# Optimization experiments

Hardware: AMD Instinct MI355X
Metric: run time of the kernel (lower is better)

Reference implementation:

```python
import jax, jax.numpy as jnp
import numpy as np


def setup_inputs() -> dict:
    key = jax.random.key(0)
    k0, k1, k2, k3, k4 = jax.random.split(key, 5)
    B, S, D, F, E = 2, 1024, 1024, 2048, 8
    x = jax.random.normal(k0, (B, S, D), dtype=jnp.float32)
    router_weight = jax.random.normal(k1, (D, E), dtype=jnp.float32) * (1.0 / np.sqrt(D))
    std_in = (1.0 / np.sqrt(3.0)) / np.sqrt(D)   # fan_in = d_model for w1/w2
    std_out = (1.0 / np.sqrt(3.0)) / np.sqrt(F)  # fan_in = d_ff for w3
    w1 = jax.random.normal(k2, (E, D, F), dtype=jnp.float32) * std_in
    w2 = jax.random.normal(k3, (E, D, F), dtype=jnp.float32) * std_in
    w3 = jax.random.normal(k4, (E, F, D), dtype=jnp.float32) * std_out
    return {"x": x, "router_weight": router_weight, "w1": w1, "w2": w2, "w3": w3, "top_k": 2}


def reference(x, router_weight, w1, w2, w3, top_k):
    B, S, D = x.shape
    E = w1.shape[0]
    xf = x.reshape(-1, D)                         # (T, D), T = B*S
    T = xf.shape[0]
    # Router: linear + softmax + top-k, then renormalize top-k weights
    logits = xf @ router_weight                   # (T, E)
    probs = jax.nn.softmax(logits, axis=-1)
    topk_w, topk_idx = jax.lax.top_k(probs, top_k)  # (T, k)
    topk_w = topk_w / jnp.sum(topk_w, axis=-1, keepdims=True)
    # Dense combine weights: cw[t, e] = routing weight if expert e selected for token t, else 0
    cw = jnp.zeros((T, E), dtype=xf.dtype).at[jnp.arange(T)[:, None], topk_idx].add(topk_w)
    # Expert SwiGLU: loop over small fixed expert count (structurally distinct weights)
    out = jnp.zeros_like(xf)
    for e in range(E):
        h = jax.nn.silu(xf @ w1[e]) * (xf @ w2[e])  # (T, F)
        out = out + cw[:, e:e + 1] * (h @ w3[e])    # (T, D)
    return out.reshape(B, S, D)
```

## Files before the change

kernel.cpp:

```cpp
#include <hip/hip_runtime.h>
#include <hip/hip_bf16.h>
#include <stdint.h>

#define T_TOK 2048
#define DMODEL 1024
#define FDIM 2048
#define NEXP 8
#define MAXS 40

typedef __bf16 bf16;
typedef __attribute__((ext_vector_type(8))) __bf16 bf16x8;
typedef __attribute__((ext_vector_type(4))) float f32x4;

#define GLOBAL_AS __attribute__((address_space(1)))
#define LDS_AS __attribute__((address_space(3)))

__global__ __launch_bounds__(64) void moe_router(
    const float* __restrict__ x, const float* __restrict__ rw,
    bf16* __restrict__ xb, int* __restrict__ counts,
    int* __restrict__ tok_list, float* __restrict__ wgt_list)
{
  const int t = blockIdx.x;
  const int lane = threadIdx.x;
  const float* xr = x + (size_t)t * DMODEL;
  bf16* xbr = xb + (size_t)t * DMODEL;
  float acc[NEXP];
#pragma unroll
  for (int e = 0; e < NEXP; ++e) acc[e] = 0.f;
  for (int d = lane; d < DMODEL; d += 64) {
    float xv = xr[d];
    xbr[d] = (bf16)xv;
    const float* r = rw + (size_t)d * NEXP;
#pragma unroll
    for (int e = 0; e < NEXP; ++e) acc[e] += xv * r[e];
  }
#pragma unroll
  for (int e = 0; e < NEXP; ++e) {
#pragma unroll
    for (int off = 32; off >= 1; off >>= 1)
      acc[e] += __shfl_xor(acc[e], off, 64);
  }
  if (lane == 0) {
    int i0 = 0; float m0 = acc[0];
#pragma unroll
    for (int e = 1; e < NEXP; ++e) { if (acc[e] > m0) { m0 = acc[e]; i0 = e; } }
    int i1 = -1; float m1 = -3.402823466e38f;
#pragma unroll
    for (int e = 0; e < NEXP; ++e) { if (e != i0 && acc[e] > m1) { m1 = acc[e]; i1 = e; } }
    float r = expf(m1 - m0);
    float w0 = 1.f / (1.f + r);
    float w1v = r / (1.f + r);
    int p0 = atomicAdd(&counts[i0], 1);
    tok_list[i0 * T_TOK + p0] = t;
    wgt_list[i0 * T_TOK + p0] = w0;
    int p1 = atomicAdd(&counts[i1], 1);
    tok_list[i1 * T_TOK + p1] = t;
    wgt_list[i1 * T_TOK + p1] = w1v;
  }
}

__global__ void moe_prefix(const int* __restrict__ counts, int* __restrict__ base,
                           int* __restrict__ sched)
{
  if (threadIdx.x == 0) {
    int s = 0, i = 0;
    for (int e = 0; e < NEXP; ++e) {
      base[e] = s; s += counts[e];
      const int nt = (counts[e] + 127) / 128;
      for (int tt = 0; tt < nt; ++tt) sched[i++] = (e << 16) | tt;
    }
    for (; i < MAXS; ++i) sched[i] = -1;
  }
}

__global__ __launch_bounds__(256) void transpose_cvt(
    const float* __restrict__ in, bf16* __restrict__ out, int R, int C)
{
  __shared__ float tile[64][65];
  const size_t slab = (size_t)R * C;
  const float* inp = in + (size_t)blockIdx.z * slab;
  bf16* outp = out + (size_t)blockIdx.z * slab;
  const int rb = blockIdx.y * 64, cb = blockIdx.x * 64;
  const int tid = threadIdx.x;
  const int r = tid >> 2, c0 = (tid & 3) * 16;
  const float* src = inp + (size_t)(rb + r) * C + (cb + c0);
#pragma unroll
  for (int j = 0; j < 16; j += 4) {
    f32x4 v = *(const f32x4*)(src + j);
    tile[r][c0 + j + 0] = v[0];
    tile[r][c0 + j + 1] = v[1];
    tile[r][c0 + j + 2] = v[2];
    tile[r][c0 + j + 3] = v[3];
  }
  __syncthreads();
  bf16x8 a, b;
#pragma unroll
  for (int j = 0; j < 8; ++j) a[j] = (bf16)tile[c0 + j][r];
#pragma unroll
  for (int j = 0; j < 8; ++j) b[j] = (bf16)tile[c0 + 8 + j][r];
  bf16* dst = outp + (size_t)(cb + r) * R + (rb + c0);
  *(bf16x8*)dst = a;
  *(bf16x8*)(dst + 8) = b;
}

__global__ __launch_bounds__(256) void moe_gemm1_fast(
    const bf16* __restrict__ xb,
    const bf16* __restrict__ w1t, const bf16* __restrict__ w2t,
    const int* __restrict__ tok_list, const int* __restrict__ counts,
    const int* __restrict__ base, const int* __restrict__ sched,
    bf16* __restrict__ H)
{
  const int s = sched[blockIdx.y];
  if (s < 0) return;
  const int e = s >> 16, tt = s & 0xffff;
  const int cnt = counts[e];
  int rem = cnt - tt * 128; if (rem > 128) rem = 128;
  if (rem <= 0) return;
  const int ft = blockIdx.x;

  __shared__ __align__(16) bf16 As[2][4][128][8];
  __shared__ __align__(16) bf16 Ws[2][2][4][64][8];
  __shared__ int toks[128];

  const int tid = threadIdx.x;
  const int lane = tid & 63;
  const int w = tid >> 6;
  const int wr = w >> 1, wc = w & 1;
  const int lh = lane >> 4, ll = lane & 15;

  if (tid < 128) {
    int r = tid < rem ? tid : rem - 1;
    toks[tid] = tok_list[e * T_TOK + tt * 128 + r];
  }
  __syncthreads();

  const int arh = w & 1;
  const int akc = w >> 1;
  const bf16* asrc = xb + (size_t)toks[arh * 64 + lane] * DMODEL;
  const bf16* w1e = w1t + ((size_t)e * FDIM + (size_t)ft * 64 + lane) * DMODEL;
  const bf16* w2e = w2t + ((size_t)e * FDIM + (size_t)ft * 64 + lane) * DMODEL;

  f32x4 acc1[4][2], acc2[4][2];
  const f32x4 fz = {0.f, 0.f, 0.f, 0.f};
#pragma unroll
  for (int mf = 0; mf < 4; ++mf)
#pragma unroll
    for (int nf = 0; nf < 2; ++nf) { acc1[mf][nf] = fz; acc2[mf][nf] = fz; }

#define STAGE1(B, K0)                                                                   \
  {                                                                                     \
    __builtin_amdgcn_global_load_lds((const GLOBAL_AS void*)(asrc + (K0) + akc * 8),    \
        (LDS_AS void*)&As[B][akc][arh * 64][0], 16, 0, 0);                              \
    __builtin_amdgcn_global_load_lds((const GLOBAL_AS void*)(asrc + (K0) + (akc + 2) * 8), \
        (LDS_AS void*)&As[B][akc + 2][arh * 64][0], 16, 0, 0);                          \
    __builtin_amdgcn_global_load_lds((const GLOBAL_AS void*)(w1e + (K0) + w * 8),       \
        (LDS_AS void*)&Ws[B][0][w][0][0], 16, 0, 0);                                    \
    __builtin_amdgcn_global_load_lds((const GLOBAL_AS void*)(w2e + (K0) + w * 8),       \
        (LDS_AS void*)&Ws[B][1][w][0][0], 16, 0, 0);                                    \
  }

  STAGE1(0, 0);
  __syncthreads();
  int cur = 0;
  for (int t = 0; t < DMODEL / 32; ++t) {
    if (t + 1 < DMODEL / 32) STAGE1(cur ^ 1, (t + 1) * 32);
    bf16x8 af[4];
#pragma unroll
    for (int mf = 0; mf < 4; ++mf)
      af[mf] = *(const bf16x8*)&As[cur][lh][wr * 64 + mf * 16 + ll][0];
    bf16x8 b1[2], b2[2];
#pragma unroll
    for (int nf = 0; nf < 2; ++nf) {
      b1[nf] = *(const bf16x8*)&Ws[cur][0][lh][wc * 32 + nf * 16 + ll][0];
      b2[nf] = *(const bf16x8*)&Ws[cur][1][lh][wc * 32 + nf * 16 + ll][0];
    }
#pragma unroll
    for (int mf = 0; mf < 4; ++mf)
#pragma unroll
      for (int nf = 0; nf < 2; ++nf) {
        acc1[mf][nf] = __builtin_amdgcn_mfma_f32_16x16x32_bf16(af[mf], b1[nf], acc1[mf][nf], 0, 0, 0);
        acc2[mf][nf] = __builtin_amdgcn_mfma_f32_16x16x32_bf16(af[mf], b2[nf], acc2[mf][nf], 0, 0, 0);
      }
    __syncthreads();
    cur ^= 1;
  }
#undef STAGE1

  const int hbase = base[e] + tt * 128;
#pragma unroll
  for (int mf = 0; mf < 4; ++mf)
#pragma unroll
    for (int nf = 0; nf < 2; ++nf)
#pragma unroll
      for (int r = 0; r < 4; ++r) {
        const int rl = wr * 64 + mf * 16 + lh * 4 + r;
        if (rl < rem) {
          const int fg = ft * 64 + wc * 32 + nf * 16 + ll;
          const float a = acc1[mf][nf][r];
          const float b = acc2[mf][nf][r];
          const float h = (a / (1.f + expf(-a))) * b;
          H[(size_t)(hbase + rl) * FDIM + fg] = (bf16)h;
        }
      }
}

__global__ __launch_bounds__(256) void moe_gemm2_fast(
    const bf16* __restrict__ H, const bf16* __restrict__ w3t,
    const int* __restrict__ tok_list, const float* __restrict__ wgt_list,
    const int* __restrict__ counts, const int* __restrict__ base,
    const int* __restrict__ sched, float* __restrict__ out)
{
  const int s = sched[blockIdx.y];
  if (s < 0) return;
  const int e = s >> 16, tt = s & 0xffff;
  const int cnt = counts[e];
  int rem = cnt - tt * 128; if (rem > 128) rem = 128;
  if (rem <= 0) return;
  const int dt = blockIdx.x;
  const int kz = blockIdx.z;

  __shared__ __align__(16) bf16 As[2][4][128][8];
  __shared__ __align__(16) bf16 Ws[2][4][64][8];
  __shared__ int toks[128];
  __shared__ float wgts[128];

  const int tid = threadIdx.x;
  const int lane = tid & 63;
  const int w = tid >> 6;
  const int wr = w >> 1, wc = w & 1;
  const int lh = lane >> 4, ll = lane & 15;

  if (tid < 128) {
    int r = tid < rem ? tid : rem - 1;
    toks[tid] = tok_list[e * T_TOK + tt * 128 + r];
    wgts[tid] = wgt_list[e * T_TOK + tt * 128 + r];
  }
  __syncthreads();

  const int hbase = base[e] + tt * 128;
  const int arh = w & 1;
  const int akc = w >> 1;
  int myrow = arh * 64 + lane; if (myrow >= rem) myrow = rem - 1;
  const bf16* asrc = H + (size_t)(hbase + myrow) * FDIM + (size_t)kz * (FDIM / 2);
  const bf16* w3e = w3t + ((size_t)e * DMODEL + (size_t)dt * 64 + lane) * FDIM + (size_t)kz * (FDIM / 2);

  f32x4 acc[4][2];
  const f32x4 fz = {0.f, 0.f, 0.f, 0.f};
#pragma unroll
  for (int mf = 0; mf < 4; ++mf)
#pragma unroll
    for (int nf = 0; nf < 2; ++nf) acc[mf][nf] = fz;

#define STAGE2(B, K0)                                                                   \
  {                                                                                     \
    __builtin_amdgcn_global_load_lds((const GLOBAL_AS void*)(asrc + (K0) + akc * 8),    \
        (LDS_AS void*)&As[B][akc][arh * 64][0], 16, 0, 0);                              \
    __builtin_amdgcn_global_load_lds((const GLOBAL_AS void*)(asrc + (K0) + (akc + 2) * 8), \
        (LDS_AS void*)&As[B][akc + 2][arh * 64][0], 16, 0, 0);                          \
    __builtin_amdgcn_global_load_lds((const GLOBAL_AS void*)(w3e + (K0) + w * 8),       \
        (LDS_AS void*)&Ws[B][w][0][0], 16, 0, 0);                                      \
  }

  STAGE2(0, 0);
  __syncthreads();
  int cur = 0;
  for (int t = 0; t < (FDIM / 2) / 32; ++t) {
    if (t + 1 < (FDIM / 2) / 32) STAGE2(cur ^ 1, (t + 1) * 32);
    bf16x8 af[4];
#pragma unroll
    for (int mf = 0; mf < 4; ++mf)
      af[mf] = *(const bf16x8*)&As[cur][lh][wr * 64 + mf * 16 + ll][0];
    bf16x8 bv[2];
#pragma unroll
    for (int nf = 0; nf < 2; ++nf)
      bv[nf] = *(const bf16x8*)&Ws[cur][lh][wc * 32 + nf * 16 + ll][0];
#pragma unroll
    for (int mf = 0; mf < 4; ++mf)
#pragma unroll
      for (int nf = 0; nf < 2; ++nf)
        acc[mf][nf] = __builtin_amdgcn_mfma_f32_16x16x32_bf16(af[mf], bv[nf], acc[mf][nf], 0, 0, 0);
    __syncthreads();
    cur ^= 1;
  }
#undef STAGE2

#pragma unroll
  for (int mf = 0; mf < 4; ++mf)
#pragma unroll
    for (int nf = 0; nf < 2; ++nf)
#pragma unroll
      for (int r = 0; r < 4; ++r) {
        const int rl = wr * 64 + mf * 16 + lh * 4 + r;
        if (rl < rem) {
          const int col = dt * 64 + wc * 32 + nf * 16 + ll;
          atomicAdd(&out[(size_t)toks[rl] * DMODEL + col], acc[mf][nf][r] * wgts[rl]);
        }
      }
}

__global__ __launch_bounds__(256, 2) void moe_gemm1(
    const bf16* __restrict__ xb,
    const float* __restrict__ w1, const float* __restrict__ w2,
    const int* __restrict__ tok_list, const int* __restrict__ counts,
    const int* __restrict__ base, bf16* __restrict__ H)
{
  const int e = blockIdx.z;
  const int tt = blockIdx.y;
  const int ft = blockIdx.x;
  const int cnt = counts[e];
  if (tt * 128 >= cnt) return;
  int rem = cnt - tt * 128; if (rem > 128) rem = 128;

  __shared__ __align__(16) bf16 As[4][128][8];
  __shared__ __align__(16) bf16 Ws[2][4][64][8];
  __shared__ int toks[128];

  const int tid = threadIdx.x;
  const int lane = tid & 63;
  const int w = tid >> 6;
  const int wr = w >> 1, wc = w & 1;
  const int lh = lane >> 4, ll = lane & 15;

  if (tid < 128) {
    int r = tid < rem ? tid : rem - 1;
    toks[tid] = tok_list[e * T_TOK + tt * 128 + r];
  }
  __syncthreads();

  f32x4 acc1[4][2], acc2[4][2];
  const f32x4 fz = {0.f, 0.f, 0.f, 0.f};
#pragma unroll
  for (int mf = 0; mf < 4; ++mf)
#pragma unroll
    for (int nf = 0; nf < 2; ++nf) { acc1[mf][nf] = fz; acc2[mf][nf] = fz; }

  const float* w1e = w1 + (size_t)e * DMODEL * FDIM + ft * 64;
  const float* w2e = w2 + (size_t)e * DMODEL * FDIM + ft * 64;
  const int sf = tid & 63;
  const int skc = tid >> 6;

  for (int k0 = 0; k0 < DMODEL; k0 += 32) {
    __syncthreads();
#pragma unroll
    for (int i = 0; i < 2; ++i) {
      const int c = w + i * 4;
      const int kc = c >> 1;
      const int rh = c & 1;
      const int row = rh * 64 + lane;
      const bf16* gp = xb + (size_t)toks[row] * DMODEL + (k0 + kc * 8);
      __builtin_amdgcn_global_load_lds((const GLOBAL_AS void*)gp,
          (LDS_AS void*)&As[kc][rh * 64][0], 16, 0, 0);
    }
    {
      const size_t rowoff = (size_t)(k0 + skc * 8) * FDIM + sf;
      const float* s1 = w1e + rowoff;
      const float* s2 = w2e + rowoff;
      bf16x8 v1, v2;
#pragma unroll
      for (int j = 0; j < 8; ++j) {
        v1[j] = (bf16)s1[(size_t)j * FDIM];
        v2[j] = (bf16)s2[(size_t)j * FDIM];
      }
      *(bf16x8*)&Ws[0][skc][sf][0] = v1;
      *(bf16x8*)&Ws[1][skc][sf][0] = v2;
    }
    __syncthreads();
    bf16x8 af[4];
#pragma unroll
    for (int mf = 0; mf < 4; ++mf)
      af[mf] = *(const bf16x8*)&As[lh][wr * 64 + mf * 16 + ll][0];
    bf16x8 b1[2], b2[2];
#pragma unroll
    for (int nf = 0; nf < 2; ++nf) {
      b1[nf] = *(const bf16x8*)&Ws[0][lh][wc * 32 + nf * 16 + ll][0];
      b2[nf] = *(const bf16x8*)&Ws[1][lh][wc * 32 + nf * 16 + ll][0];
    }
#pragma unroll
    for (int mf = 0; mf < 4; ++mf)
#pragma unroll
      for (int nf = 0; nf < 2; ++nf) {
        acc1[mf][nf] = __builtin_amdgcn_mfma_f32_16x16x32_bf16(af[mf], b1[nf], acc1[mf][nf], 0, 0, 0);
        acc2[mf][nf] = __builtin_amdgcn_mfma_f32_16x16x32_bf16(af[mf], b2[nf], acc2[mf][nf], 0, 0, 0);
      }
  }

  const int hbase = base[e] + tt * 128;
#pragma unroll
  for (int mf = 0; mf < 4; ++mf)
#pragma unroll
    for (int nf = 0; nf < 2; ++nf)
#pragma unroll
      for (int r = 0; r < 4; ++r) {
        const int rl = wr * 64 + mf * 16 + lh * 4 + r;
        if (rl < rem) {
          const int fg = ft * 64 + wc * 32 + nf * 16 + ll;
          const float a = acc1[mf][nf][r];
          const float b = acc2[mf][nf][r];
          const float h = (a / (1.f + expf(-a))) * b;
          H[(size_t)(hbase + rl) * FDIM + fg] = (bf16)h;
        }
      }
}

__global__ __launch_bounds__(256, 2) void moe_gemm2(
    const bf16* __restrict__ H, const float* __restrict__ w3,
    const int* __restrict__ tok_list, const float* __restrict__ wgt_list,
    const int* __restrict__ counts, const int* __restrict__ base,
    float* __restrict__ out)
{
  const int e = blockIdx.z;
  const int tt = blockIdx.y;
  const int dt = blockIdx.x;
  const int cnt = counts[e];
  if (tt * 128 >= cnt) return;
  int rem = cnt - tt * 128; if (rem > 128) rem = 128;

  __shared__ __align__(16) bf16 As[4][128][8];
  __shared__ __align__(16) bf16 Ws[4][64][8];
  __shared__ int toks[128];
  __shared__ float wgts[128];

  const int tid = threadIdx.x;
  const int lane = tid & 63;
  const int w = tid >> 6;
  const int wr = w >> 1, wc = w & 1;
  const int lh = lane >> 4, ll = lane & 15;

  if (tid < 128) {
    int r = tid < rem ? tid : rem - 1;
    toks[tid] = tok_list[e * T_TOK + tt * 128 + r];
    wgts[tid] = wgt_list[e * T_TOK + tt * 128 + r];
  }
  __syncthreads();

  f32x4 acc[4][2];
  const f32x4 fz = {0.f, 0.f, 0.f, 0.f};
#pragma unroll
  for (int mf = 0; mf < 4; ++mf)
#pragma unroll
    for (int nf = 0; nf < 2; ++nf) acc[mf][nf] = fz;

  const int hbase = base[e] + tt * 128;
  const float* w3e = w3 + (size_t)e * FDIM * DMODEL + dt * 64;
  const int sf = tid & 63;
  const int skc = tid >> 6;

  for (int k0 = 0; k0 < FDIM; k0 += 32) {
    __syncthreads();
#pragma unroll
    for (int i = 0; i < 2; ++i) {
      const int c = w + i * 4;
      const int kc = c >> 1;
      const int rh = c & 1;
      int row = rh * 64 + lane;
      if (row >= rem) row = rem - 1;
      const bf16* gp = H + (size_t)(hbase + row) * FDIM + (k0 + kc * 8);
      __builtin_amdgcn_global_load_lds((const GLOBAL_AS void*)gp,
          (LDS_AS void*)&As[kc][rh * 64][0], 16, 0, 0);
    }
    {
      const size_t rowoff = (size_t)(k0 + skc * 8) * DMODEL + sf;
      const float* s3 = w3e + rowoff;
      bf16x8 v;
#pragma unroll
      for (int j = 0; j < 8; ++j) v[j] = (bf16)s3[(size_t)j * DMODEL];
      *(bf16x8*)&Ws[skc][sf][0] = v;
    }
    __syncthreads();
    bf16x8 af[4];
#pragma unroll
    for (int mf = 0; mf < 4; ++mf)
      af[mf] = *(const bf16x8*)&As[lh][wr * 64 + mf * 16 + ll][0];
    bf16x8 bv[2];
#pragma unroll
    for (int nf = 0; nf < 2; ++nf)
      bv[nf] = *(const bf16x8*)&Ws[lh][wc * 32 + nf * 16 + ll][0];
#pragma unroll
    for (int mf = 0; mf < 4; ++mf)
#pragma unroll
      for (int nf = 0; nf < 2; ++nf)
        acc[mf][nf] = __builtin_amdgcn_mfma_f32_16x16x32_bf16(af[mf], bv[nf], acc[mf][nf], 0, 0, 0);
  }

#pragma unroll
  for (int mf = 0; mf < 4; ++mf)
#pragma unroll
    for (int nf = 0; nf < 2; ++nf)
#pragma unroll
      for (int r = 0; r < 4; ++r) {
        const int rl = wr * 64 + mf * 16 + lh * 4 + r;
        if (rl < rem) {
          const int col = dt * 64 + wc * 32 + nf * 16 + ll;
          atomicAdd(&out[(size_t)toks[rl] * DMODEL + col], acc[mf][nf][r] * wgts[rl]);
        }
      }
}

extern "C" void kernel_launch(void* const* d_in, const int* in_sizes, int n_in,
                              void* d_out, int out_size, void* d_ws, size_t ws_size,
                              hipStream_t stream)
{
  const float* x  = (const float*)d_in[0];
  const float* rw = (const float*)d_in[1];
  const float* w1 = (const float*)d_in[2];
  const float* w2 = (const float*)d_in[3];
  const float* w3 = (const float*)d_in[4];
  float* out = (float*)d_out;
  char* ws = (char*)d_ws;

  size_t off = 0;
  auto take = [&](size_t bytes) -> char* {
    char* p = ws + off;
    off = (off + bytes + 255) & ~(size_t)255;
    return p;
  };
  bf16* xb        = (bf16*)take((size_t)T_TOK * DMODEL * sizeof(bf16));
  bf16* H         = (bf16*)take((size_t)2 * T_TOK * FDIM * sizeof(bf16));
  int* tok_list   = (int*)take((size_t)NEXP * T_TOK * sizeof(int));
  float* wgt_list = (float*)take((size_t)NEXP * T_TOK * sizeof(float));
  int* counts     = (int*)take(64);
  int* base       = (int*)take(64);
  int* sched      = (int*)take(MAXS * sizeof(int));
  bf16* w1t       = (bf16*)take((size_t)NEXP * DMODEL * FDIM * sizeof(bf16));
  bf16* w2t       = (bf16*)take((size_t)NEXP * DMODEL * FDIM * sizeof(bf16));
  bf16* w3t       = (bf16*)take((size_t)NEXP * FDIM * DMODEL * sizeof(bf16));
  const bool fast = (ws_size >= off);

  hipMemsetAsync(d_out, 0, (size_t)out_size * sizeof(float), stream);
  hipMemsetAsync(counts, 0, NEXP * sizeof(int), stream);

  moe_router<<<dim3(T_TOK), dim3(64), 0, stream>>>(x, rw, xb, counts, tok_list, wgt_list);
  moe_prefix<<<dim3(1), dim3(64), 0, stream>>>(counts, base, sched);

  if (fast) {
    transpose_cvt<<<dim3(FDIM / 64, DMODEL / 64, NEXP), dim3(256), 0, stream>>>(w1, w1t, DMODEL, FDIM);
    transpose_cvt<<<dim3(FDIM / 64, DMODEL / 64, NEXP), dim3(256), 0, stream>>>(w2, w2t, DMODEL, FDIM);
    transpose_cvt<<<dim3(DMODEL / 64, FDIM / 64, NEXP), dim3(256), 0, stream>>>(w3, w3t, FDIM, DMODEL);
    moe_gemm1_fast<<<dim3(FDIM / 64, MAXS), dim3(256), 0, stream>>>(
        xb, w1t, w2t, tok_list, counts, base, sched, H);
    moe_gemm2_fast<<<dim3(DMODEL / 64, MAXS, 2), dim3(256), 0, stream>>>(
        H, w3t, tok_list, wgt_list, counts, base, sched, out);
  } else {
    moe_gemm1<<<dim3(FDIM / 64, T_TOK / 128, NEXP), dim3(256), 0, stream>>>(
        xb, w1, w2, tok_list, counts, base, H);
    moe_gemm2<<<dim3(DMODEL / 64, T_TOK / 128, NEXP), dim3(256), 0, stream>>>(
        H, w3, tok_list, wgt_list, counts, base, out);
  }
}
```

Measured before the change: 305.5 us.

## Deepen LDS pipelines with vmcnt waits and merge w1/w2 transpose launches

```diff
diff --git a/kernel.cpp b/kernel.cpp
--- a/kernel.cpp
+++ b/kernel.cpp
@@ -14,6 +14,8 @@
 
 #define GLOBAL_AS __attribute__((address_space(1)))
 #define LDS_AS __attribute__((address_space(3)))
+
+#define VMCNT(n) asm volatile("s_waitcnt vmcnt(" #n ")" ::: "memory")
 
 __global__ __launch_bounds__(64) void moe_router(
     const float* __restrict__ x, const float* __restrict__ rw,
@@ -73,6 +75,40 @@
   }
 }
 
+__global__ __launch_bounds__(256) void transpose_cvt12(
+    const float* __restrict__ w1, const float* __restrict__ w2,
+    bf16* __restrict__ w1t, bf16* __restrict__ w2t)
+{
+  const int R = DMODEL, C = FDIM;
+  __shared__ float tile[64][65];
+  const int z = blockIdx.z;
+  const int e = z & 7;
+  const size_t slab = (size_t)R * C;
+  const float* inp = (z < 8 ? w1 : w2) + (size_t)e * slab;
+  bf16* outp = (z < 8 ? w1t : w2t) + (size_t)e * slab;
+  const int rb = blockIdx.y * 64, cb = blockIdx.x * 64;
+  const int tid = threadIdx.x;
+  const int r = tid >> 2, c0 = (tid & 3) * 16;
+  const float* src = inp + (size_t)(rb + r) * C + (cb + c0);
+#pragma unroll
+  for (int j = 0; j < 16; j += 4) {
+    f32x4 v = *(const f32x4*)(src + j);
+    tile[r][c0 + j + 0] = v[0];
+    tile[r][c0 + j + 1] = v[1];
+    tile[r][c0 + j + 2] = v[2];
+    tile[r][c0 + j + 3] = v[3];
+  }
+  __syncthreads();
+  bf16x8 a, b;
+#pragma unroll
+  for (int j = 0; j < 8; ++j) a[j] = (bf16)tile[c0 + j][r];
+#pragma unroll
+  for (int j = 0; j < 8; ++j) b[j] = (bf16)tile[c0 + 8 + j][r];
+  bf16* dst = outp + (size_t)(cb + r) * R + (rb + c0);
+  *(bf16x8*)dst = a;
+  *(bf16x8*)(dst + 8) = b;
+}
+
 __global__ __launch_bounds__(256) void transpose_cvt(
     const float* __restrict__ in, bf16* __restrict__ out, int R, int C)
 {
@@ -118,8 +154,8 @@
   if (rem <= 0) return;
   const int ft = blockIdx.x;
 
-  __shared__ __align__(16) bf16 As[2][4][128][8];
-  __shared__ __align__(16) bf16 Ws[2][2][4][64][8];
+  __shared__ __align__(16) bf16 As[3][4][128][8];
+  __shared__ __align__(16) bf16 Ws[3][2][4][64][8];
   __shared__ int toks[128];
 
   const int tid = threadIdx.x;
@@ -159,21 +195,27 @@
         (LDS_AS void*)&Ws[B][1][w][0][0], 16, 0, 0);                                    \
   }
 
+  const int NT = DMODEL / 32;
   STAGE1(0, 0);
-  __syncthreads();
-  int cur = 0;
-  for (int t = 0; t < DMODEL / 32; ++t) {
-    if (t + 1 < DMODEL / 32) STAGE1(cur ^ 1, (t + 1) * 32);
-    bf16x8 af[4];
-#pragma unroll
-    for (int mf = 0; mf < 4; ++mf)
-      af[mf] = *(const bf16x8*)&As[cur][lh][wr * 64 + mf * 16 + ll][0];
-    bf16x8 b1[2], b2[2];
+  STAGE1(1, 32);
+  VMCNT(4);
+  __builtin_amdgcn_s_barrier();
+
+  int ld = 0;
+  for (int t = 0; t < NT; ++t) {
+    int pf = ld + 2; if (pf >= 3) pf -= 3;
+    if (t + 2 < NT) STAGE1(pf, (t + 2) * 32);
+
+    bf16x8 af[4], b1[2], b2[2];
+#pragma unroll
+    for (int mf = 0; mf < 4; ++mf)
+      af[mf] = *(const bf16x8*)&As[ld][lh][wr * 64 + mf * 16 + ll][0];
 #pragma unroll
     for (int nf = 0; nf < 2; ++nf) {
-      b1[nf] = *(const bf16x8*)&Ws[cur][0][lh][wc * 32 + nf * 16 + ll][0];
-      b2[nf] = *(const bf16x8*)&Ws[cur][1][lh][wc * 32 + nf * 16 + ll][0];
-    }
+      b1[nf] = *(const bf16x8*)&Ws[ld][0][lh][wc * 32 + nf * 16 + ll][0];
+      b2[nf] = *(const bf16x8*)&Ws[ld][1][lh][wc * 32 + nf * 16 + ll][0];
+    }
+    __builtin_amdgcn_s_setprio(1);
 #pragma unroll
     for (int mf = 0; mf < 4; ++mf)
 #pragma unroll
@@ -181,8 +223,16 @@
         acc1[mf][nf] = __builtin_amdgcn_mfma_f32_16x16x32_bf16(af[mf], b1[nf], acc1[mf][nf], 0, 0, 0);
         acc2[mf][nf] = __builtin_amdgcn_mfma_f32_16x16x32_bf16(af[mf], b2[nf], acc2[mf][nf], 0, 0, 0);
       }
-    __syncthreads();
-    cur ^= 1;
+    __builtin_amdgcn_s_setprio(0);
+
+    if (t + 2 < NT) {
+      VMCNT(4);
+      __builtin_amdgcn_s_barrier();
+    } else if (t + 1 < NT) {
+      VMCNT(0);
+      __builtin_amdgcn_s_barrier();
+    }
+    ld = (ld + 1 == 3) ? 0 : ld + 1;
   }
 #undef STAGE1
 
@@ -219,8 +269,8 @@
   const int dt = blockIdx.x;
   const int kz = blockIdx.z;
 
-  __shared__ __align__(16) bf16 As[2][4][128][8];
-  __shared__ __align__(16) bf16 Ws[2][4][64][8];
+  __shared__ __align__(16) bf16 As[4][4][128][8];
+  __shared__ __align__(16) bf16 Ws[4][4][64][8];
   __shared__ int toks[128];
   __shared__ float wgts[128];
 
@@ -261,26 +311,44 @@
         (LDS_AS void*)&Ws[B][w][0][0], 16, 0, 0);                                      \
   }
 
+  const int NT = (FDIM / 2) / 32;
   STAGE2(0, 0);
-  __syncthreads();
-  int cur = 0;
-  for (int t = 0; t < (FDIM / 2) / 32; ++t) {
-    if (t + 1 < (FDIM / 2) / 32) STAGE2(cur ^ 1, (t + 1) * 32);
-    bf16x8 af[4];
-#pragma unroll
-    for (int mf = 0; mf < 4; ++mf)
-      af[mf] = *(const bf16x8*)&As[cur][lh][wr * 64 + mf * 16 + ll][0];
-    bf16x8 bv[2];
+  STAGE2(1, 32);
+  STAGE2(2, 64);
+  VMCNT(6);
+  __builtin_amdgcn_s_barrier();
+
+  int ld = 0;
+  for (int t = 0; t < NT; ++t) {
+    int pf = ld + 3; if (pf >= 4) pf -= 4;
+    if (t + 3 < NT) STAGE2(pf, (t + 3) * 32);
+
+    bf16x8 af[4], bv[2];
+#pragma unroll
+    for (int mf = 0; mf < 4; ++mf)
+      af[mf] = *(const bf16x8*)&As[ld][lh][wr * 64 + mf * 16 + ll][0];
 #pragma unroll
     for (int nf = 0; nf < 2; ++nf)
-      bv[nf] = *(const bf16x8*)&Ws[cur][lh][wc * 32 + nf * 16 + ll][0];
+      bv[nf] = *(const bf16x8*)&Ws[ld][lh][wc * 32 + nf * 16 + ll][0];
+    __builtin_amdgcn_s_setprio(1);
 #pragma unroll
     for (int mf = 0; mf < 4; ++mf)
 #pragma unroll
       for (int nf = 0; nf < 2; ++nf)
         acc[mf][nf] = __builtin_amdgcn_mfma_f32_16x16x32_bf16(af[mf], bv[nf], acc[mf][nf], 0, 0, 0);
-    __syncthreads();
-    cur ^= 1;
+    __builtin_amdgcn_s_setprio(0);
+
+    if (t + 3 < NT) {
+      VMCNT(6);
+      __builtin_amdgcn_s_barrier();
+    } else if (t + 2 < NT) {
+      VMCNT(3);
+      __builtin_amdgcn_s_barrier();
+    } else if (t + 1 < NT) {
+      VMCNT(0);
+      __builtin_amdgcn_s_barrier();
+    }
+    ld = (ld + 1 == 4) ? 0 : ld + 1;
   }
 #undef STAGE2
 
@@ -533,8 +601,7 @@
   moe_prefix<<<dim3(1), dim3(64), 0, stream>>>(counts, base, sched);
 
   if (fast) {
-    transpose_cvt<<<dim3(FDIM / 64, DMODEL / 64, NEXP), dim3(256), 0, stream>>>(w1, w1t, DMODEL, FDIM);
-    transpose_cvt<<<dim3(FDIM / 64, DMODEL / 64, NEXP), dim3(256), 0, stream>>>(w2, w2t, DMODEL, FDIM);
+    transpose_cvt12<<<dim3(FDIM / 64, DMODEL / 64, 2 * NEXP), dim3(256), 0, stream>>>(w1, w2, w1t, w2t);
     transpose_cvt<<<dim3(DMODEL / 64, FDIM / 64, NEXP), dim3(256), 0, stream>>>(w3, w3t, FDIM, DMODEL);
     moe_gemm1_fast<<<dim3(FDIM / 64, MAXS), dim3(256), 0, stream>>>(
         xb, w1t, w2t, tok_list, counts, base, sched, H);
```

Measured after the change: 303.1 us. About the same (-0.8%).
